# Kernel optimization log

Hardware: AMD Instinct MI355X
Metric: run time of the kernel (lower is better)

The kernel has to match this reference:

```python
import jax, jax.numpy as jnp
import numpy as np

N_NODES = 100000
N_FEAT = 512
HIDDEN = 256
N_CLASSES = 40
N_EDGES = 1600000
K = 10
ALPHA = 0.1


def setup_inputs() -> dict:
    key = jax.random.key(0)
    ks = jax.random.split(key, 8)
    feat = jax.random.normal(ks[0], (N_NODES, N_FEAT), dtype=jnp.float32)
    src = jax.random.randint(ks[1], (N_EDGES,), 0, N_NODES, dtype=jnp.int32)
    dst = jax.random.randint(ks[2], (N_EDGES,), 0, N_NODES, dtype=jnp.int32)
    # linear layers (PyTorch-style uniform init)
    s1 = 1.0 / np.sqrt(N_FEAT)
    W1 = jax.random.uniform(ks[3], (N_FEAT, HIDDEN), minval=-s1, maxval=s1, dtype=jnp.float32)
    b1 = jax.random.uniform(ks[4], (HIDDEN,), minval=-s1, maxval=s1, dtype=jnp.float32)
    s2 = 1.0 / np.sqrt(HIDDEN)
    W2 = jax.random.uniform(ks[5], (HIDDEN, N_CLASSES), minval=-s2, maxval=s2, dtype=jnp.float32)
    b2 = jax.random.uniform(ks[6], (N_CLASSES,), minval=-s2, maxval=s2, dtype=jnp.float32)
    # PPR init for per-hop weights: temp[k] = alpha*(1-alpha)^k, temp[K] = (1-alpha)^K
    temp = ALPHA * (1.0 - ALPHA) ** np.arange(K + 1)
    temp[-1] = (1.0 - ALPHA) ** K
    temp = jnp.asarray(temp, dtype=jnp.float32)
    return {"feat": feat, "W1": W1, "b1": b1, "W2": W2, "b2": b2,
            "temp": temp, "src": src, "dst": dst}


def reference(feat, W1, b1, W2, b2, temp, src, dst):
    N = feat.shape[0]
    # dgl.add_self_loop
    loop = jnp.arange(N, dtype=src.dtype)
    src_f = jnp.concatenate([src, loop])
    dst_f = jnp.concatenate([dst, loop])
    # MLP: lin1 -> relu -> lin2 (dropout is identity at inference)
    h = jax.nn.relu(feat @ W1 + b1) @ W2 + b2  # [N, C]
    # symmetric normalization: norm_e = d[dst] * d[src], d = deg^{-1/2}
    deg = jax.ops.segment_sum(jnp.ones_like(dst_f, dtype=h.dtype), dst_f, num_segments=N)
    d = jax.lax.rsqrt(deg)  # deg >= 1 due to self loops
    norm = (d[dst_f] * d[src_f])[:, None]  # [E, 1]
    # K-hop propagation with learned per-hop weights
    TH = h * temp[0]
    for k in range(K):
        msg = h[src_f] * norm                     # gather + edge scale
        h = jax.ops.segment_sum(msg, dst_f, num_segments=N)  # scatter-sum
        TH = TH + h * temp[k + 1]
    return jax.nn.log_softmax(TH, axis=1)
```

## Files before the change

### kernel.cpp

```cpp
#include <hip/hip_runtime.h>
#include <math.h>

#define N_NODES 100000
#define N_FEAT  512
#define HIDDEN  256
#define N_CLS   40
#define N_EDGES 1600000
#define K_HOPS  10
#define SCAN_BLOCKS 98
#define HPAD 64

typedef __attribute__((ext_vector_type(8))) short short8;
typedef __attribute__((ext_vector_type(4))) float f4_t;

__device__ __forceinline__ short f2bf(float f) {
    union { float f; unsigned u; } x; x.f = f;
    unsigned r = x.u + 0x7fffu + ((x.u >> 16) & 1u);
    return (short)(r >> 16);
}

__device__ __forceinline__ float bf2f(short b) {
    union { unsigned u; float f; } x;
    x.u = ((unsigned)(unsigned short)b) << 16;
    return x.f;
}


__global__ __launch_bounds__(256) void init_deg_kernel(int* __restrict__ deg) {
    int v = blockIdx.x * 256 + threadIdx.x;
    if (v < N_NODES) deg[v] = 1;
}

__global__ __launch_bounds__(256) void count_dst_kernel(const int* __restrict__ dst,
                                                        int* __restrict__ deg) {
    int e = blockIdx.x * 256 + threadIdx.x;
    if (e < N_EDGES) atomicAdd(&deg[dst[e]], 1);
}

__global__ __launch_bounds__(256) void rsqrt_deg_kernel(const int* __restrict__ deg,
                                                        float* __restrict__ d) {
    int v = blockIdx.x * 256 + threadIdx.x;
    if (v < N_NODES) d[v] = rsqrtf((float)deg[v]);
}


__global__ __launch_bounds__(1024) void scan_partial_kernel(const int* __restrict__ deg,
                                                            int* __restrict__ blocksum) {
    __shared__ int s[1024];
    int t = threadIdx.x;
    int idx = blockIdx.x * 1024 + t;
    s[t] = (idx < N_NODES) ? deg[idx] : 0;
    __syncthreads();
#pragma unroll
    for (int off = 512; off > 0; off >>= 1) {
        if (t < off) s[t] += s[t + off];
        __syncthreads();
    }
    if (t == 0) blocksum[blockIdx.x] = s[0];
}

__global__ __launch_bounds__(64) void scan_blocks_kernel(const int* __restrict__ blocksum,
                                                         int* __restrict__ blockoff) {
    if (threadIdx.x == 0) {
        int run = 0;
        for (int b = 0; b < SCAN_BLOCKS; ++b) { blockoff[b] = run; run += blocksum[b]; }
    }
}

__global__ __launch_bounds__(1024) void scan_write_kernel(const int* __restrict__ deg,
                                                          const int* __restrict__ blockoff,
                                                          int* __restrict__ rowptr,
                                                          int* __restrict__ cursor) {
    __shared__ int s[1024];
    int t = threadIdx.x;
    int idx = blockIdx.x * 1024 + t;
    int v = (idx < N_NODES) ? deg[idx] : 0;
    s[t] = v;
    __syncthreads();
#pragma unroll
    for (int off = 1; off < 1024; off <<= 1) {
        int add = (t >= off) ? s[t - off] : 0;
        __syncthreads();
        s[t] += add;
        __syncthreads();
    }
    int pre = s[t] - v + blockoff[blockIdx.x];
    if (idx <= N_NODES) rowptr[idx] = pre;
    if (idx < N_NODES) cursor[idx] = pre;
}

__global__ __launch_bounds__(256) void scatter_edges_kernel(const int* __restrict__ src,
                                                            const int* __restrict__ dst,
                                                            const float* __restrict__ d,
                                                            int* __restrict__ cursor,
                                                            int2* __restrict__ epair) {
    int e = blockIdx.x * 256 + threadIdx.x;
    if (e >= N_EDGES) return;
    int u = src[e], v = dst[e];
    int pos = atomicAdd(&cursor[v], 1);
    int2 p;
    p.x = u;
    p.y = __float_as_int(d[u] * d[v]);
    epair[pos] = p;
}

__global__ __launch_bounds__(256) void scatter_self_kernel(const float* __restrict__ d,
                                                           int* __restrict__ cursor,
                                                           int2* __restrict__ epair) {
    int v = blockIdx.x * 256 + threadIdx.x;
    if (v >= N_NODES) return;
    int pos = atomicAdd(&cursor[v], 1);
    float dv = d[v];
    int2 p;
    p.x = v;
    p.y = __float_as_int(dv * dv);
    epair[pos] = p;
}

__global__ __launch_bounds__(256) void cvt_w1_kernel(const float* __restrict__ W1,
                                                     short* __restrict__ W1T) {
    int lin = blockIdx.x * 256 + threadIdx.x;
    int k = lin >> 8, n = lin & 255;
    W1T[n * 512 + k] = f2bf(W1[lin]);
}

__global__ __launch_bounds__(256) void cvt_w2_kernel(const float* __restrict__ W2,
                                                     short* __restrict__ W2T) {
    int lin = blockIdx.x * 256 + threadIdx.x;
    int n = lin >> 8, k = lin & 255;
    W2T[lin] = (n < N_CLS) ? f2bf(W2[k * N_CLS + n]) : (short)0;
}

__global__ __launch_bounds__(256) void mlp_kernel(const float* __restrict__ feat,
                                                  const short* __restrict__ W1T,
                                                  const float* __restrict__ b1,
                                                  const short* __restrict__ W2T,
                                                  const float* __restrict__ b2,
                                                  const float* __restrict__ temp,
                                                  short* __restrict__ h,
                                                  float* __restrict__ TH) {
    __shared__ union {
        struct { short A[64][72]; short B[256][72]; } a;
        short W2s[48][264];
    } uS;
    __shared__ short sH[64][264];

    const int tid = threadIdx.x;
    const int rbase = blockIdx.x * 64;
    const int lane = tid & 63;
    const int wv = tid >> 6;
    const int quad = lane >> 4;
    const int l15 = lane & 15;

    f4_t acc[4][4];
#pragma unroll
    for (int m = 0; m < 4; ++m)
#pragma unroll
        for (int n = 0; n < 4; ++n) acc[m][n] = (f4_t)0.f;

    const int arow = tid >> 2;
    const int akq = tid & 3;
    for (int kt = 0; kt < 8; ++kt) {
        __syncthreads();
        {
            int grow = rbase + arow;
            f4_t f0 = (f4_t)0.f, f1 = (f4_t)0.f, f2 = (f4_t)0.f, f3 = (f4_t)0.f;
            if (grow < N_NODES) {
                const f4_t* p = (const f4_t*)(feat + grow * N_FEAT + kt * 64 + akq * 16);
                f0 = p[0]; f1 = p[1]; f2 = p[2]; f3 = p[3];
            }
            short8 lo, hi;
            lo[0]=f2bf(f0[0]); lo[1]=f2bf(f0[1]); lo[2]=f2bf(f0[2]); lo[3]=f2bf(f0[3]);
            lo[4]=f2bf(f1[0]); lo[5]=f2bf(f1[1]); lo[6]=f2bf(f1[2]); lo[7]=f2bf(f1[3]);
            hi[0]=f2bf(f2[0]); hi[1]=f2bf(f2[1]); hi[2]=f2bf(f2[2]); hi[3]=f2bf(f2[3]);
            hi[4]=f2bf(f3[0]); hi[5]=f2bf(f3[1]); hi[6]=f2bf(f3[2]); hi[7]=f2bf(f3[3]);
            short8* dstp = (short8*)&uS.a.A[arow][akq * 16];
            dstp[0] = lo; dstp[1] = hi;
        }
#pragma unroll
        for (int p = 0; p < 8; ++p) {
            int lin = p * 256 + tid;
            int col = lin >> 3, kc = lin & 7;
            *(short8*)&uS.a.B[col][kc * 8] =
                *(const short8*)(W1T + col * 512 + kt * 64 + kc * 8);
        }
        __syncthreads();
#pragma unroll
        for (int kk = 0; kk < 64; kk += 32) {
            short8 af[4], bf[4];
#pragma unroll
            for (int m = 0; m < 4; ++m)
                af[m] = *(const short8*)&uS.a.A[m * 16 + l15][kk + quad * 8];
#pragma unroll
            for (int n = 0; n < 4; ++n)
                bf[n] = *(const short8*)&uS.a.B[wv * 64 + n * 16 + l15][kk + quad * 8];
#pragma unroll
            for (int m = 0; m < 4; ++m)
#pragma unroll
                for (int n = 0; n < 4; ++n)
                    acc[m][n] = __builtin_amdgcn_mfma_f32_16x16x32_bf16(af[m], bf[n],
                                                                        acc[m][n], 0, 0, 0);
        }
    }
    __syncthreads();

#pragma unroll
    for (int n = 0; n < 4; ++n) {
        int col = wv * 64 + n * 16 + l15;
        float bb = b1[col];
#pragma unroll
        for (int m = 0; m < 4; ++m)
#pragma unroll
            for (int r = 0; r < 4; ++r) {
                float v = acc[m][n][r] + bb;
                sH[m * 16 + quad * 4 + r][col] = f2bf(v > 0.f ? v : 0.f);
            }
    }
#pragma unroll
    for (int p = 0; p < 6; ++p) {
        int lin = p * 256 + tid;
        int n = lin >> 5, kc = lin & 31;
        *(short8*)&uS.W2s[n][kc * 8] = *(const short8*)(W2T + n * 256 + kc * 8);
    }
    __syncthreads();

    f4_t accB[3];
#pragma unroll
    for (int n = 0; n < 3; ++n) accB[n] = (f4_t)0.f;
#pragma unroll
    for (int kk = 0; kk < 256; kk += 32) {
        short8 a = *(const short8*)&sH[wv * 16 + l15][kk + quad * 8];
#pragma unroll
        for (int n = 0; n < 3; ++n) {
            short8 b = *(const short8*)&uS.W2s[n * 16 + l15][kk + quad * 8];
            accB[n] = __builtin_amdgcn_mfma_f32_16x16x32_bf16(a, b, accB[n], 0, 0, 0);
        }
    }
    float t0 = temp[0];
#pragma unroll
    for (int n = 0; n < 3; ++n) {
        int col = n * 16 + l15;
        if (col < N_CLS) {
            float bb = b2[col];
#pragma unroll
            for (int r = 0; r < 4; ++r) {
                int grow = rbase + wv * 16 + quad * 4 + r;
                if (grow < N_NODES) {
                    float v = accB[n][r] + bb;
                    h[grow * HPAD + col] = f2bf(v);
                    TH[grow * N_CLS + col] = t0 * v;
                }
            }
        }
    }
}

__global__ __launch_bounds__(256) void prop_kernel(const short* __restrict__ h,
                                                   short* __restrict__ hn,
                                                   const int* __restrict__ rowptr,
                                                   const int2* __restrict__ epair,
                                                   float* __restrict__ TH,
                                                   const float* __restrict__ temp,
                                                   int kidx) {
    int gid = blockIdx.x * 256 + threadIdx.x;
    int v = gid / 5;
    if (v >= N_NODES) return;
    int c = gid - v * 5;
    int s = rowptr[v], e = rowptr[v + 1];
    f4_t a0 = (f4_t)0.f, a1 = (f4_t)0.f;
    int j = s;
    for (; j + 4 <= e; j += 4) {
        int2 e0 = epair[j], e1 = epair[j + 1], e2 = epair[j + 2], e3 = epair[j + 3];
        short8 h0 = *(const short8*)(h + e0.x * HPAD + c * 8);
        short8 h1 = *(const short8*)(h + e1.x * HPAD + c * 8);
        short8 h2 = *(const short8*)(h + e2.x * HPAD + c * 8);
        short8 h3 = *(const short8*)(h + e3.x * HPAD + c * 8);
        float w0 = __int_as_float(e0.y), w1 = __int_as_float(e1.y);
        float w2 = __int_as_float(e2.y), w3 = __int_as_float(e3.y);
#pragma unroll
        for (int i = 0; i < 4; ++i) {
            a0[i] += w0 * bf2f(h0[i]) + w1 * bf2f(h1[i]) + w2 * bf2f(h2[i]) + w3 * bf2f(h3[i]);
            a1[i] += w0 * bf2f(h0[4 + i]) + w1 * bf2f(h1[4 + i]) + w2 * bf2f(h2[4 + i]) +
                     w3 * bf2f(h3[4 + i]);
        }
    }
    for (; j < e; ++j) {
        int2 ep = epair[j];
        short8 hb = *(const short8*)(h + ep.x * HPAD + c * 8);
        float w = __int_as_float(ep.y);
#pragma unroll
        for (int i = 0; i < 4; ++i) {
            a0[i] += w * bf2f(hb[i]);
            a1[i] += w * bf2f(hb[4 + i]);
        }
    }
    float tk = temp[kidx];
    short8 ob;
#pragma unroll
    for (int i = 0; i < 4; ++i) { ob[i] = f2bf(a0[i]); ob[4 + i] = f2bf(a1[i]); }
    *(short8*)(hn + v * HPAD + c * 8) = ob;
    f4_t* pt = (f4_t*)(TH + v * N_CLS + c * 8);
    pt[0] += tk * a0;
    pt[1] += tk * a1;
}

__global__ __launch_bounds__(256) void lsm_kernel(float* __restrict__ out) {
    int wid = (blockIdx.x * 256 + threadIdx.x) >> 6;
    int lane = threadIdx.x & 63;
    if (wid >= N_NODES) return;
    float x = (lane < N_CLS) ? out[wid * N_CLS + lane] : -INFINITY;
    float m = x;
#pragma unroll
    for (int o = 32; o > 0; o >>= 1) m = fmaxf(m, __shfl_xor(m, o, 64));
    float e = (lane < N_CLS) ? expf(x - m) : 0.f;
    float s = e;
#pragma unroll
    for (int o = 32; o > 0; o >>= 1) s += __shfl_xor(s, o, 64);
    float r = x - m - logf(s);
    if (lane < N_CLS) out[wid * N_CLS + lane] = r;
}


extern "C" void kernel_launch(void* const* d_in, const int* in_sizes, int n_in,
                              void* d_out, int out_size, void* d_ws, size_t ws_size,
                              hipStream_t stream) {
    const float* feat = (const float*)d_in[0];
    const float* W1   = (const float*)d_in[1];
    const float* b1   = (const float*)d_in[2];
    const float* W2   = (const float*)d_in[3];
    const float* b2   = (const float*)d_in[4];
    const float* temp = (const float*)d_in[5];
    const int*   src  = (const int*)d_in[6];
    const int*   dst  = (const int*)d_in[7];
    float* out = (float*)d_out;

    char* ws = (char*)d_ws;
    int*   deg    = (int*)(ws + 0);
    short* W1T    = (short*)(ws + 0);
    short* W2T    = (short*)(ws + 262144);
    float* dnorm  = (float*)(ws + 400000);
    int*   rowptr = (int*)(ws + 800000);
    int*   cursor = (int*)(ws + 1200016);
    int2*  epair  = (int2*)(ws + 1600032);
    short* h0     = (short*)(ws + 15200032);
    short* h1     = (short*)(ws + 28000032);
    int*   blocksum = (int*)(ws + 40800032);
    int*   blockoff = (int*)(ws + 40800432);

    init_deg_kernel<<<(N_NODES + 255) / 256, 256, 0, stream>>>(deg);
    count_dst_kernel<<<(N_EDGES + 255) / 256, 256, 0, stream>>>(dst, deg);
    rsqrt_deg_kernel<<<(N_NODES + 255) / 256, 256, 0, stream>>>(deg, dnorm);
    scan_partial_kernel<<<SCAN_BLOCKS, 1024, 0, stream>>>(deg, blocksum);
    scan_blocks_kernel<<<1, 64, 0, stream>>>(blocksum, blockoff);
    scan_write_kernel<<<SCAN_BLOCKS, 1024, 0, stream>>>(deg, blockoff, rowptr, cursor);
    cvt_w1_kernel<<<512, 256, 0, stream>>>(W1, W1T);
    cvt_w2_kernel<<<64, 256, 0, stream>>>(W2, W2T);
    scatter_edges_kernel<<<(N_EDGES + 255) / 256, 256, 0, stream>>>(src, dst, dnorm, cursor,
                                                                    epair);
    scatter_self_kernel<<<(N_NODES + 255) / 256, 256, 0, stream>>>(dnorm, cursor, epair);

    mlp_kernel<<<(N_NODES + 63) / 64, 256, 0, stream>>>(feat, W1T, b1, W2T, b2, temp, h0, out);

    short* hc = h0;
    short* hn = h1;
    for (int k = 0; k < K_HOPS; ++k) {
        prop_kernel<<<(N_NODES * 5 + 255) / 256, 256, 0, stream>>>(hc, hn, rowptr, epair,
                                                                   out, temp, k + 1);
        short* t = hc; hc = hn; hn = t;
    }

    lsm_kernel<<<(N_NODES / 4), 256, 0, stream>>>(out);
}
```

Measured before the change: 897.5 us.

## Use chunk-major feature layout with XCD-aware block mapping in propagation

The propagated features move from a padded row-major [N,64] layout to five chunk-major planes of 8 bf16 per node. Prop blocks are remapped so each feature chunk is handled by blocks on the same XCD, keeping that chunk's 1.6MB plane resident in the local L2 during the random gathers. TH updates now use nontemporal loads and stores. The MLP kernel also drops LDS staging of W1/W2 in favour of direct global reads and software-prefetches the next feat tile into a double-buffered A tile, which trades LDS traffic for more global and L2 loads.

```diff
diff --git a/kernel.cpp b/kernel.cpp
--- a/kernel.cpp
+++ b/kernel.cpp
@@ -8,7 +8,13 @@
 #define N_EDGES 1600000
 #define K_HOPS  10
 #define SCAN_BLOCKS 98
-#define HPAD 64
+
+#define NCHUNK  5
+#define CHSTRIDE (N_NODES * 8)
+#define NBLKN   391
+#define PUNITS  (NCHUNK * NBLKN)
+#define PUPX    245
+#define PGRID   (8 * PUPX)
 
 typedef __attribute__((ext_vector_type(8))) short short8;
 typedef __attribute__((ext_vector_type(4))) float f4_t;
@@ -131,18 +137,15 @@
     W2T[lin] = (n < N_CLS) ? f2bf(W2[k * N_CLS + n]) : (short)0;
 }
 
-__global__ __launch_bounds__(256) void mlp_kernel(const float* __restrict__ feat,
-                                                  const short* __restrict__ W1T,
-                                                  const float* __restrict__ b1,
-                                                  const short* __restrict__ W2T,
-                                                  const float* __restrict__ b2,
-                                                  const float* __restrict__ temp,
-                                                  short* __restrict__ h,
-                                                  float* __restrict__ TH) {
-    __shared__ union {
-        struct { short A[64][72]; short B[256][72]; } a;
-        short W2s[48][264];
-    } uS;
+__global__ __launch_bounds__(256, 3) void mlp_kernel(const float* __restrict__ feat,
+                                                     const short* __restrict__ W1T,
+                                                     const float* __restrict__ b1,
+                                                     const short* __restrict__ W2T,
+                                                     const float* __restrict__ b2,
+                                                     const float* __restrict__ temp,
+                                                     short* __restrict__ h,
+                                                     float* __restrict__ TH) {
+    __shared__ short A[2][64][72];
     __shared__ short sH[64][264];
 
     const int tid = threadIdx.x;
@@ -160,40 +163,42 @@
 
     const int arow = tid >> 2;
     const int akq = tid & 3;
+    const int grow = rbase + arow;
+    const bool rv = (grow < N_NODES);
+    const float* fp = feat + (size_t)(rv ? grow : 0) * N_FEAT + akq * 16;
+
+    f4_t f0 = (f4_t)0.f, f1 = (f4_t)0.f, f2 = (f4_t)0.f, f3 = (f4_t)0.f;
+    if (rv) {
+        const f4_t* p = (const f4_t*)fp;
+        f0 = p[0]; f1 = p[1]; f2 = p[2]; f3 = p[3];
+    }
+
     for (int kt = 0; kt < 8; ++kt) {
-        __syncthreads();
         {
-            int grow = rbase + arow;
-            f4_t f0 = (f4_t)0.f, f1 = (f4_t)0.f, f2 = (f4_t)0.f, f3 = (f4_t)0.f;
-            if (grow < N_NODES) {
-                const f4_t* p = (const f4_t*)(feat + grow * N_FEAT + kt * 64 + akq * 16);
-                f0 = p[0]; f1 = p[1]; f2 = p[2]; f3 = p[3];
-            }
             short8 lo, hi;
             lo[0]=f2bf(f0[0]); lo[1]=f2bf(f0[1]); lo[2]=f2bf(f0[2]); lo[3]=f2bf(f0[3]);
             lo[4]=f2bf(f1[0]); lo[5]=f2bf(f1[1]); lo[6]=f2bf(f1[2]); lo[7]=f2bf(f1[3]);
             hi[0]=f2bf(f2[0]); hi[1]=f2bf(f2[1]); hi[2]=f2bf(f2[2]); hi[3]=f2bf(f2[3]);
             hi[4]=f2bf(f3[0]); hi[5]=f2bf(f3[1]); hi[6]=f2bf(f3[2]); hi[7]=f2bf(f3[3]);
-            short8* dstp = (short8*)&uS.a.A[arow][akq * 16];
+            short8* dstp = (short8*)&A[kt & 1][arow][akq * 16];
             dstp[0] = lo; dstp[1] = hi;
         }
-#pragma unroll
-        for (int p = 0; p < 8; ++p) {
-            int lin = p * 256 + tid;
-            int col = lin >> 3, kc = lin & 7;
-            *(short8*)&uS.a.B[col][kc * 8] =
-                *(const short8*)(W1T + col * 512 + kt * 64 + kc * 8);
-        }
         __syncthreads();
+        if (kt < 7 && rv) {
+            const f4_t* p = (const f4_t*)(fp + (kt + 1) * 64);
+            f0 = p[0]; f1 = p[1]; f2 = p[2]; f3 = p[3];
+        }
+        const short* wb = W1T + kt * 64;
 #pragma unroll
         for (int kk = 0; kk < 64; kk += 32) {
             short8 af[4], bf[4];
 #pragma unroll
             for (int m = 0; m < 4; ++m)
-                af[m] = *(const short8*)&uS.a.A[m * 16 + l15][kk + quad * 8];
+                af[m] = *(const short8*)&A[kt & 1][m * 16 + l15][kk + quad * 8];
 #pragma unroll
             for (int n = 0; n < 4; ++n)
-                bf[n] = *(const short8*)&uS.a.B[wv * 64 + n * 16 + l15][kk + quad * 8];
+                bf[n] = *(const short8*)(wb + (wv * 64 + n * 16 + l15) * 512 +
+                                         kk + quad * 8);
 #pragma unroll
             for (int m = 0; m < 4; ++m)
 #pragma unroll
@@ -202,7 +207,6 @@
                                                                         acc[m][n], 0, 0, 0);
         }
     }
-    __syncthreads();
 
 #pragma unroll
     for (int n = 0; n < 4; ++n) {
@@ -216,12 +220,6 @@
                 sH[m * 16 + quad * 4 + r][col] = f2bf(v > 0.f ? v : 0.f);
             }
     }
-#pragma unroll
-    for (int p = 0; p < 6; ++p) {
-        int lin = p * 256 + tid;
-        int n = lin >> 5, kc = lin & 31;
-        *(short8*)&uS.W2s[n][kc * 8] = *(const short8*)(W2T + n * 256 + kc * 8);
-    }
     __syncthreads();
 
     f4_t accB[3];
@@ -232,7 +230,7 @@
         short8 a = *(const short8*)&sH[wv * 16 + l15][kk + quad * 8];
 #pragma unroll
         for (int n = 0; n < 3; ++n) {
-            short8 b = *(const short8*)&uS.W2s[n * 16 + l15][kk + quad * 8];
+            short8 b = *(const short8*)(W2T + (n * 16 + l15) * 256 + kk + quad * 8);
             accB[n] = __builtin_amdgcn_mfma_f32_16x16x32_bf16(a, b, accB[n], 0, 0, 0);
         }
     }
@@ -242,66 +240,77 @@
         int col = n * 16 + l15;
         if (col < N_CLS) {
             float bb = b2[col];
+            int c = col >> 3, jj = col & 7;
 #pragma unroll
             for (int r = 0; r < 4; ++r) {
-                int grow = rbase + wv * 16 + quad * 4 + r;
-                if (grow < N_NODES) {
+                int grow2 = rbase + wv * 16 + quad * 4 + r;
+                if (grow2 < N_NODES) {
                     float v = accB[n][r] + bb;
-                    h[grow * HPAD + col] = f2bf(v);
-                    TH[grow * N_CLS + col] = t0 * v;
+                    h[((size_t)c * N_NODES + grow2) * 8 + jj] = f2bf(v);
+                    TH[grow2 * N_CLS + col] = t0 * v;
                 }
             }
         }
     }
 }
 
-__global__ __launch_bounds__(256) void prop_kernel(const short* __restrict__ h,
-                                                   short* __restrict__ hn,
-                                                   const int* __restrict__ rowptr,
-                                                   const int2* __restrict__ epair,
-                                                   float* __restrict__ TH,
-                                                   const float* __restrict__ temp,
-                                                   int kidx) {
-    int gid = blockIdx.x * 256 + threadIdx.x;
-    int v = gid / 5;
+__global__ __launch_bounds__(256, 8) void prop_kernel(const short* __restrict__ h,
+                                                      short* __restrict__ hn,
+                                                      const int* __restrict__ rowptr,
+                                                      const int2* __restrict__ epair,
+                                                      float* __restrict__ TH,
+                                                      const float* __restrict__ temp,
+                                                      int kidx) {
+    int bid = blockIdx.x;
+    int u = (bid & 7) * PUPX + (bid >> 3);
+    if (u >= PUNITS) return;
+    int c = u / NBLKN;
+    int nb = u - c * NBLKN;
+    int v = nb * 256 + threadIdx.x;
     if (v >= N_NODES) return;
-    int c = gid - v * 5;
+
     int s = rowptr[v], e = rowptr[v + 1];
+    const short* hb = h + (size_t)c * CHSTRIDE;
     f4_t a0 = (f4_t)0.f, a1 = (f4_t)0.f;
     int j = s;
     for (; j + 4 <= e; j += 4) {
         int2 e0 = epair[j], e1 = epair[j + 1], e2 = epair[j + 2], e3 = epair[j + 3];
-        short8 h0 = *(const short8*)(h + e0.x * HPAD + c * 8);
-        short8 h1 = *(const short8*)(h + e1.x * HPAD + c * 8);
-        short8 h2 = *(const short8*)(h + e2.x * HPAD + c * 8);
-        short8 h3 = *(const short8*)(h + e3.x * HPAD + c * 8);
+        short8 h0 = *(const short8*)(hb + (size_t)e0.x * 8);
+        short8 h1 = *(const short8*)(hb + (size_t)e1.x * 8);
+        short8 h2 = *(const short8*)(hb + (size_t)e2.x * 8);
+        short8 h3 = *(const short8*)(hb + (size_t)e3.x * 8);
         float w0 = __int_as_float(e0.y), w1 = __int_as_float(e1.y);
         float w2 = __int_as_float(e2.y), w3 = __int_as_float(e3.y);
 #pragma unroll
         for (int i = 0; i < 4; ++i) {
-            a0[i] += w0 * bf2f(h0[i]) + w1 * bf2f(h1[i]) + w2 * bf2f(h2[i]) + w3 * bf2f(h3[i]);
+            a0[i] += w0 * bf2f(h0[i]) + w1 * bf2f(h1[i]) + w2 * bf2f(h2[i]) +
+                     w3 * bf2f(h3[i]);
             a1[i] += w0 * bf2f(h0[4 + i]) + w1 * bf2f(h1[4 + i]) + w2 * bf2f(h2[4 + i]) +
                      w3 * bf2f(h3[4 + i]);
         }
     }
     for (; j < e; ++j) {
         int2 ep = epair[j];
-        short8 hb = *(const short8*)(h + ep.x * HPAD + c * 8);
+        short8 hb8 = *(const short8*)(hb + (size_t)ep.x * 8);
         float w = __int_as_float(ep.y);
 #pragma unroll
         for (int i = 0; i < 4; ++i) {
-            a0[i] += w * bf2f(hb[i]);
-            a1[i] += w * bf2f(hb[4 + i]);
+            a0[i] += w * bf2f(hb8[i]);
+            a1[i] += w * bf2f(hb8[4 + i]);
         }
     }
     float tk = temp[kidx];
     short8 ob;
 #pragma unroll
     for (int i = 0; i < 4; ++i) { ob[i] = f2bf(a0[i]); ob[4 + i] = f2bf(a1[i]); }
-    *(short8*)(hn + v * HPAD + c * 8) = ob;
-    f4_t* pt = (f4_t*)(TH + v * N_CLS + c * 8);
-    pt[0] += tk * a0;
-    pt[1] += tk * a1;
+    *(short8*)(hn + (size_t)c * CHSTRIDE + (size_t)v * 8) = ob;
+    float* pt = TH + (size_t)v * N_CLS + c * 8;
+    f4_t t0 = __builtin_nontemporal_load((const f4_t*)pt);
+    f4_t t1 = __builtin_nontemporal_load(((const f4_t*)pt) + 1);
+    t0 += tk * a0;
+    t1 += tk * a1;
+    __builtin_nontemporal_store(t0, (f4_t*)pt);
+    __builtin_nontemporal_store(t1, ((f4_t*)pt) + 1);
 }
 
 __global__ __launch_bounds__(256) void lsm_kernel(float* __restrict__ out) {
@@ -343,9 +352,9 @@
     int*   cursor = (int*)(ws + 1200016);
     int2*  epair  = (int2*)(ws + 1600032);
     short* h0     = (short*)(ws + 15200032);
-    short* h1     = (short*)(ws + 28000032);
-    int*   blocksum = (int*)(ws + 40800032);
-    int*   blockoff = (int*)(ws + 40800432);
+    short* h1     = (short*)(ws + 23200032);
+    int*   blocksum = (int*)(ws + 31200032);
+    int*   blockoff = (int*)(ws + 31200432);
 
     init_deg_kernel<<<(N_NODES + 255) / 256, 256, 0, stream>>>(deg);
     count_dst_kernel<<<(N_EDGES + 255) / 256, 256, 0, stream>>>(dst, deg);
@@ -364,8 +373,7 @@
     short* hc = h0;
     short* hn = h1;
     for (int k = 0; k < K_HOPS; ++k) {
-        prop_kernel<<<(N_NODES * 5 + 255) / 256, 256, 0, stream>>>(hc, hn, rowptr, epair,
-                                                                   out, temp, k + 1);
+        prop_kernel<<<PGRID, 256, 0, stream>>>(hc, hn, rowptr, epair, out, temp, k + 1);
         short* t = hc; hc = hn; hn = t;
     }
 
```

After: 1.387 ms. +54.6%, slower.
